# Kernel optimization log

Measured on AMD Instinct MI355X. Metric: run time of the kernel, lower is better.

The kernel has to match this reference:

```python
import jax, jax.numpy as jnp
import numpy as np

DIM = 2048
N_HEADS = 16
HEAD_DIM = DIM // N_HEADS
HIDDEN = 8192
BATCH = 2
SEQ = 2048
EPS = 1e-6


def setup_inputs() -> dict:
    key = jax.random.key(0)
    ks = jax.random.split(key, 10)
    x = jax.random.normal(ks[0], (BATCH, SEQ, DIM), dtype=jnp.float32)
    # standard RoPE angles: theta_j = 10000^{-2j/head_dim}, angle = pos * theta_j
    inv_freq = 1.0 / (10000.0 ** (np.arange(0, HEAD_DIM, 2, dtype=np.float32) / HEAD_DIM))
    angles = np.arange(SEQ, dtype=np.float32)[:, None] * inv_freq[None, :]  # [S, HD/2]
    freqs_cos = jnp.asarray(np.cos(angles))
    freqs_sin = jnp.asarray(np.sin(angles))
    # causal mask added to scores
    mask = jnp.where(jnp.tril(jnp.ones((SEQ, SEQ), dtype=bool)), 0.0, -jnp.inf)[None, None].astype(jnp.float32)
    s = 0.02
    wq = jax.random.normal(ks[1], (DIM, DIM), jnp.float32) * s
    wk = jax.random.normal(ks[2], (DIM, DIM), jnp.float32) * s
    wv = jax.random.normal(ks[3], (DIM, DIM), jnp.float32) * s
    wo = jax.random.normal(ks[4], (DIM, DIM), jnp.float32) * s
    w1 = jax.random.normal(ks[5], (DIM, HIDDEN), jnp.float32) * s
    w2 = jax.random.normal(ks[6], (HIDDEN, DIM), jnp.float32) * s
    w3 = jax.random.normal(ks[7], (DIM, HIDDEN), jnp.float32) * s
    attn_norm_w = jnp.ones((DIM,), jnp.float32)
    ffn_norm_w = jnp.ones((DIM,), jnp.float32)
    return {"x": x, "freqs_cos": freqs_cos, "freqs_sin": freqs_sin, "mask": mask,
            "wq": wq, "wk": wk, "wv": wv, "wo": wo, "w1": w1, "w2": w2, "w3": w3,
            "attn_norm_w": attn_norm_w, "ffn_norm_w": ffn_norm_w}


def _rmsnorm(x, w):
    xf = x.astype(jnp.float32)
    y = xf * jax.lax.rsqrt(jnp.mean(xf * xf, axis=-1, keepdims=True) + EPS)
    return y.astype(x.dtype) * w


def _rope(t, cos, sin):
    # t: [B,S,H,HD]; complex mult on adjacent pairs
    tr = t.astype(jnp.float32).reshape(*t.shape[:-1], HEAD_DIM // 2, 2)
    a, b = tr[..., 0], tr[..., 1]
    c = cos[None, :, None, :]  # [1,S,1,HD/2]
    s = sin[None, :, None, :]
    out = jnp.stack([a * c - b * s, a * s + b * c], axis=-1)
    return out.reshape(t.shape).astype(t.dtype)


def reference(x, freqs_cos, freqs_sin, mask, wq, wk, wv, wo, w1, w2, w3, attn_norm_w, ffn_norm_w):
    B, S, D = x.shape
    xn = _rmsnorm(x, attn_norm_w)
    q = (xn @ wq).reshape(B, S, N_HEADS, HEAD_DIM)
    k = (xn @ wk).reshape(B, S, N_HEADS, HEAD_DIM)
    v = (xn @ wv).reshape(B, S, N_HEADS, HEAD_DIM)
    q = _rope(q, freqs_cos, freqs_sin)
    k = _rope(k, freqs_cos, freqs_sin)
    scale = 1.0 / jnp.sqrt(jnp.float32(HEAD_DIM))
    scores = jnp.einsum('bqhd,bkhd->bhqk', q, k) * scale + mask
    probs = jax.nn.softmax(scores.astype(jnp.float32), axis=-1).astype(q.dtype)
    attn = jnp.einsum('bhqk,bkhd->bqhd', probs, v).reshape(B, S, D)
    h = x + attn @ wo
    hn = _rmsnorm(h, ffn_norm_w)
    ff = (jax.nn.silu(hn @ w1) * (hn @ w3)) @ w2
    return h + ff
```

## Files before the change

### kernel.cpp

```cpp
#include <hip/hip_runtime.h>
#include <cmath>

#define DIM    2048
#define NHEADS 16
#define HD     128
#define HIDDEN 8192
#define SEQ    2048
#define MTOK   4096
#define EPS    1e-6f

typedef __bf16 bf16;
typedef __bf16 bf16x8 __attribute__((ext_vector_type(8)));
typedef __bf16 bf16x4 __attribute__((ext_vector_type(4)));
typedef float  f32x4  __attribute__((ext_vector_type(4)));

typedef __attribute__((address_space(1))) const void gvoid_t;
typedef __attribute__((address_space(3))) void lvoid_t;

__global__ void k_transpose4(const float* __restrict__ in0, const float* __restrict__ in1,
                             const float* __restrict__ in2, const float* __restrict__ in3,
                             bf16* __restrict__ o0, bf16* __restrict__ o1,
                             bf16* __restrict__ o2, bf16* __restrict__ o3,
                             int R, int C) {
    __shared__ float tile[64][65];
    const float* in = blockIdx.z == 0 ? in0 : blockIdx.z == 1 ? in1 : blockIdx.z == 2 ? in2 : in3;
    bf16* out       = blockIdx.z == 0 ? o0  : blockIdx.z == 1 ? o1  : blockIdx.z == 2 ? o2  : o3;
    int r0 = blockIdx.y * 64, c0 = blockIdx.x * 64;
    int tx = threadIdx.x, ty = threadIdx.y;
#pragma unroll
    for (int i = ty; i < 64; i += 4)
        tile[i][tx] = in[(size_t)(r0 + i) * C + (c0 + tx)];
    __syncthreads();
#pragma unroll
    for (int i = ty; i < 64; i += 4)
        out[(size_t)(c0 + i) * R + (r0 + tx)] = (bf16)tile[tx][i];
}

__global__ void k_rmsnorm(const float* __restrict__ x, const float* __restrict__ w,
                          bf16* __restrict__ out) {
    int row = blockIdx.x;
    int tid = threadIdx.x;
    const float4* xr = (const float4*)(x + (size_t)row * DIM);
    float4 a = xr[tid];
    float4 b = xr[tid + 256];
    float ss = a.x*a.x + a.y*a.y + a.z*a.z + a.w*a.w
             + b.x*b.x + b.y*b.y + b.z*b.z + b.w*b.w;
#pragma unroll
    for (int off = 32; off > 0; off >>= 1) ss += __shfl_down(ss, off, 64);
    __shared__ float red[4];
    if ((tid & 63) == 0) red[tid >> 6] = ss;
    __syncthreads();
    float tot = red[0] + red[1] + red[2] + red[3];
    float inv = rsqrtf(tot * (1.0f / DIM) + EPS);
    const float4* wr = (const float4*)w;
    float4 w0 = wr[tid], w1 = wr[tid + 256];
    bf16x4* o = (bf16x4*)(out + (size_t)row * DIM);
    bf16x4 v0, v1;
    v0[0] = (bf16)(a.x * inv * w0.x); v0[1] = (bf16)(a.y * inv * w0.y);
    v0[2] = (bf16)(a.z * inv * w0.z); v0[3] = (bf16)(a.w * inv * w0.w);
    v1[0] = (bf16)(b.x * inv * w1.x); v1[1] = (bf16)(b.y * inv * w1.y);
    v1[2] = (bf16)(b.z * inv * w1.z); v1[3] = (bf16)(b.w * inv * w1.w);
    o[tid] = v0;
    o[tid + 256] = v1;
}

template<int CFG, int MODE>
__global__ __launch_bounds__(512, 2) void k2b(
    const bf16* __restrict__ A, const bf16* __restrict__ B1,
    const bf16* __restrict__ B2, const float* __restrict__ resid,
    const float* __restrict__ fcos, const float* __restrict__ fsin,
    bf16* __restrict__ oq, bf16* __restrict__ ok, bf16* __restrict__ ov,
    float* __restrict__ of, int N, int K)
{
    constexpr int  BN   = (CFG == 0) ? 256 : 128;
    constexpr int  WN   = (CFG == 0) ? 4 : 2;
    constexpr int  WM   = 8 / WN;
    constexpr int  MFR  = (256 / WM) / 16;
    constexpr bool DUAL = (CFG == 1);
    constexpr int  NH   = (CFG == 2) ? 3 : 4;
    constexpr uint32_t SLOT = (uint32_t)NH * 16384u;

    __shared__ __align__(16) char lds[2 * NH * 16384];

    const int tid  = threadIdx.x;
    const int wid  = tid >> 6;
    const int lane = tid & 63;
    const int quad = lane >> 4;
    const int l16  = lane & 15;
    const int wm   = wid / WN;
    const int wn   = wid % WN;
    const int m0   = blockIdx.y * 256;
    const int n0   = blockIdx.x * BN;
    const int NT   = K >> 6;

    const uint32_t swz0 = (uint32_t)((quad ^ (l16 & 7)) << 4);
    const uint32_t swz1 = (uint32_t)(((4 + quad) ^ (l16 & 7)) << 4);
    const uint32_t a_base  = (uint32_t)((wm * (256 / WM) + l16) * 128);
    const uint32_t b_base  = 32768u + (uint32_t)((wn * 64 + l16) * 128);

    auto stage = [&](int H, int Tt) {
        const uint32_t lb = (uint32_t)(Tt & 1) * SLOT + (uint32_t)H * 16384u
                          + (uint32_t)wid * 1024u;
        const int k0 = Tt << 6;
        const bf16* gb; int grow;
        if (H < 2) { gb = A; grow = m0 + H * 128; }
        else if constexpr (CFG == 0) { gb = B1; grow = n0 + (H - 2) * 128; }
        else if constexpr (CFG == 1) { gb = (H == 2) ? B1 : B2; grow = n0; }
        else { gb = B1; grow = n0; }
#pragma unroll
        for (int rho = 0; rho < 2; ++rho) {
            const int r  = (tid >> 3) + rho * 64;
            const int sp = (tid & 7) ^ (r & 7);
            const bf16* g = gb + (size_t)(grow + r) * K + k0 + sp * 8;
            __builtin_amdgcn_global_load_lds((gvoid_t*)g,
                (lvoid_t*)&lds[lb + (uint32_t)rho * 8192u], 16, 0, 0);
        }
    };

    f32x4 acc1[MFR][4] = {};
    f32x4 acc2[DUAL ? MFR : 1][4] = {};

#pragma unroll
    for (int h = 0; h < NH; ++h) stage(h, 0);
#pragma unroll
    for (int h = 0; h < NH; ++h) stage(h, 1);
    if constexpr (NH == 4) asm volatile("s_waitcnt vmcnt(8)" ::: "memory");
    else                   asm volatile("s_waitcnt vmcnt(6)" ::: "memory");
    __builtin_amdgcn_s_barrier();

    for (int T = 0; T < NT; ++T) {
        const uint32_t sb = (uint32_t)(T & 1) * SLOT;

#pragma unroll
        for (int ks = 0; ks < 2; ++ks) {
            const uint32_t sw = ks ? swz1 : swz0;
            bf16x8 af[MFR], bf1[4], bf2[DUAL ? 4 : 1];
#pragma unroll
            for (int mi = 0; mi < MFR; ++mi)
                af[mi] = *(const bf16x8*)&lds[sb + a_base + (uint32_t)mi * 2048u + sw];
#pragma unroll
            for (int ni = 0; ni < 4; ++ni)
                bf1[ni] = *(const bf16x8*)&lds[sb + b_base + (uint32_t)ni * 2048u + sw];
            if constexpr (DUAL)
#pragma unroll
                for (int ni = 0; ni < 4; ++ni)
                    bf2[ni] = *(const bf16x8*)&lds[sb + b_base + 16384u
                                                   + (uint32_t)ni * 2048u + sw];
            __builtin_amdgcn_s_setprio(1);
#pragma unroll
            for (int mi = 0; mi < MFR; ++mi)
#pragma unroll
                for (int ni = 0; ni < 4; ++ni) {
                    acc1[mi][ni] = __builtin_amdgcn_mfma_f32_16x16x32_bf16(
                        af[mi], bf1[ni], acc1[mi][ni], 0, 0, 0);
                    if constexpr (DUAL)
                        acc2[mi][ni] = __builtin_amdgcn_mfma_f32_16x16x32_bf16(
                            af[mi], bf2[ni], acc2[mi][ni], 0, 0, 0);
                }
            __builtin_amdgcn_s_setprio(0);
        }

        __builtin_amdgcn_s_barrier();

        if (T + 2 < NT) {
#pragma unroll
            for (int h = 0; h < NH; ++h) stage(h, T + 2);
        }
        if (T + 1 < NT) {
            if (T + 2 < NT) {
                if constexpr (NH == 4) asm volatile("s_waitcnt vmcnt(8)" ::: "memory");
                else                   asm volatile("s_waitcnt vmcnt(6)" ::: "memory");
            } else {
                asm volatile("s_waitcnt vmcnt(0)" ::: "memory");
            }
        }
        __builtin_amdgcn_s_barrier();
    }

    if constexpr (MODE == 1) {
        const int region = n0 >> 11;
        bf16* dst = region == 0 ? oq : (region == 1 ? ok : ov);
        const int c0 = (n0 & 2047) + wn * 64;
#pragma unroll
        for (int mi = 0; mi < MFR; ++mi)
#pragma unroll
            for (int i = 0; i < 4; ++i) {
                int row = m0 + wm * 128 + mi * 16 + quad * 4 + i;
                int pos = row & (SEQ - 1);
#pragma unroll
                for (int ni = 0; ni < 4; ++ni) {
                    int c = c0 + ni * 16 + l16;
                    float vA = acc1[mi][ni][i];
                    if (region < 2) {
                        float vB = __shfl_xor(vA, 1, 64);
                        int fi = (c & 127) >> 1;
                        float cs = fcos[pos * 64 + fi], sn = fsin[pos * 64 + fi];
                        vA = (l16 & 1) ? (vB * sn + vA * cs) : (vA * cs - vB * sn);
                    }
                    dst[(size_t)row * DIM + c] = (bf16)vA;
                }
            }
    } else if constexpr (MODE == 3) {
#pragma unroll
        for (int mi = 0; mi < MFR; ++mi)
#pragma unroll
            for (int i = 0; i < 4; ++i) {
                int row = m0 + wm * 64 + mi * 16 + quad * 4 + i;
#pragma unroll
                for (int ni = 0; ni < 4; ++ni) {
                    int col = n0 + wn * 64 + ni * 16 + l16;
                    float v1 = acc1[mi][ni][i];
                    float v2 = acc2[mi][ni][i];
                    float g = v1 / (1.0f + __expf(-v1));
                    oq[(size_t)row * (size_t)N + col] = (bf16)(g * v2);
                }
            }
    } else {
#pragma unroll
        for (int mi = 0; mi < MFR; ++mi)
#pragma unroll
            for (int i = 0; i < 4; ++i) {
                int row = m0 + wm * 64 + mi * 16 + quad * 4 + i;
#pragma unroll
                for (int ni = 0; ni < 4; ++ni) {
                    int col = n0 + wn * 64 + ni * 16 + l16;
                    of[(size_t)row * N + col] = resid[(size_t)row * N + col]
                                              + acc1[mi][ni][i];
                }
            }
    }
}

__global__ __launch_bounds__(256, 2) void k_flash(
    const bf16* __restrict__ q, const bf16* __restrict__ k,
    const bf16* __restrict__ v, bf16* __restrict__ o)
{
    const int qt = 15 - blockIdx.x;
    const int bh = blockIdx.y;
    const int b  = bh >> 4, h = bh & 15;
    const int tid  = threadIdx.x;
    const int wid  = tid >> 6, lane = tid & 63;
    const int quad = lane >> 4, l16 = lane & 15;

    __shared__ bf16 Ks [128][136];
    __shared__ bf16 Vts[128][136];

    const int q0 = qt * 128;
    const size_t baseQ  = ((size_t)b * SEQ + q0) * DIM + (size_t)h * HD;
    const size_t baseKV = ((size_t)b * SEQ) * DIM + (size_t)h * HD;

    bf16x8 qf[2][4];
#pragma unroll
    for (int mi = 0; mi < 2; ++mi)
#pragma unroll
        for (int ks = 0; ks < 4; ++ks)
            qf[mi][ks] = *(const bf16x8*)&q[baseQ +
                (size_t)(wid * 32 + mi * 16 + l16) * DIM + ks * 32 + quad * 8];

    f32x4 acc_o[2][8] = {};
    float m_run[2][4], l_run[2][4];
#pragma unroll
    for (int mi = 0; mi < 2; ++mi)
#pragma unroll
        for (int i = 0; i < 4; ++i) { m_run[mi][i] = -INFINITY; l_run[mi][i] = 0.f; }

    const float scale = 0.08838834764831845f;
    const int krow = tid >> 1, kcol = (tid & 1) * 64;

    for (int kt = 0; kt <= qt; ++kt) {
        const int kbase = kt * 128;
        __syncthreads();
#pragma unroll
        for (int j = 0; j < 8; ++j)
            *(uint4*)&Ks[krow][kcol + j * 8] =
                *(const uint4*)&k[baseKV + (size_t)(kbase + krow) * DIM + kcol + j * 8];
#pragma unroll
        for (int j = 0; j < 8; ++j) {
            bf16x8 vv = *(const bf16x8*)&v[baseKV + (size_t)(kbase + krow) * DIM + kcol + j * 8];
#pragma unroll
            for (int e = 0; e < 8; ++e)
                Vts[kcol + j * 8 + e][krow] = vv[e];
        }
        __syncthreads();

        f32x4 accs[2][8] = {};
#pragma unroll
        for (int ks = 0; ks < 4; ++ks)
#pragma unroll
            for (int ni = 0; ni < 8; ++ni) {
                bf16x8 kf = *(const bf16x8*)&Ks[ni * 16 + l16][ks * 32 + quad * 8];
#pragma unroll
                for (int mi = 0; mi < 2; ++mi)
                    accs[mi][ni] = __builtin_amdgcn_mfma_f32_16x16x32_bf16(
                        qf[mi][ks], kf, accs[mi][ni], 0, 0, 0);
            }

#pragma unroll
        for (int mi = 0; mi < 2; ++mi)
#pragma unroll
            for (int i = 0; i < 4; ++i) {
                int grow = q0 + wid * 32 + mi * 16 + quad * 4 + i;
                float mx = -INFINITY;
#pragma unroll
                for (int ni = 0; ni < 8; ++ni) {
                    float sv = accs[mi][ni][i] * scale;
                    int col = kbase + ni * 16 + l16;
                    if (col > grow) sv = -INFINITY;
                    accs[mi][ni][i] = sv;
                    mx = fmaxf(mx, sv);
                }
                mx = fmaxf(mx, __shfl_xor(mx, 1, 64));
                mx = fmaxf(mx, __shfl_xor(mx, 2, 64));
                mx = fmaxf(mx, __shfl_xor(mx, 4, 64));
                mx = fmaxf(mx, __shfl_xor(mx, 8, 64));
                float mnew  = fmaxf(m_run[mi][i], mx);
                float alpha = __expf(m_run[mi][i] - mnew);
                m_run[mi][i] = mnew;
                float rsum = 0.f;
#pragma unroll
                for (int ni = 0; ni < 8; ++ni) {
                    float p = __expf(accs[mi][ni][i] - mnew);
                    accs[mi][ni][i] = p;
                    rsum += p;
                }
                rsum += __shfl_xor(rsum, 1, 64);
                rsum += __shfl_xor(rsum, 2, 64);
                rsum += __shfl_xor(rsum, 4, 64);
                rsum += __shfl_xor(rsum, 8, 64);
                l_run[mi][i] = l_run[mi][i] * alpha + rsum;
#pragma unroll
                for (int ni = 0; ni < 8; ++ni) acc_o[mi][ni][i] *= alpha;
            }

        __syncthreads();
#pragma unroll
        for (int mi = 0; mi < 2; ++mi)
#pragma unroll
            for (int ni = 0; ni < 8; ++ni)
#pragma unroll
                for (int i = 0; i < 4; ++i)
                    Ks[wid * 32 + mi * 16 + quad * 4 + i][ni * 16 + l16] =
                        (bf16)accs[mi][ni][i];
        __syncthreads();

#pragma unroll
        for (int ks2 = 0; ks2 < 4; ++ks2) {
            bf16x8 pf[2];
#pragma unroll
            for (int mi = 0; mi < 2; ++mi)
                pf[mi] = *(const bf16x8*)&Ks[wid * 32 + mi * 16 + l16][ks2 * 32 + quad * 8];
#pragma unroll
            for (int ni = 0; ni < 8; ++ni) {
                bf16x8 vf = *(const bf16x8*)&Vts[ni * 16 + l16][ks2 * 32 + quad * 8];
#pragma unroll
                for (int mi = 0; mi < 2; ++mi)
                    acc_o[mi][ni] = __builtin_amdgcn_mfma_f32_16x16x32_bf16(
                        pf[mi], vf, acc_o[mi][ni], 0, 0, 0);
            }
        }
    }

#pragma unroll
    for (int mi = 0; mi < 2; ++mi)
#pragma unroll
        for (int i = 0; i < 4; ++i) {
            float invl = 1.0f / l_run[mi][i];
            int row = q0 + wid * 32 + mi * 16 + quad * 4 + i;
            size_t rb = ((size_t)b * SEQ + row) * DIM + (size_t)h * HD;
#pragma unroll
            for (int ni = 0; ni < 8; ++ni)
                o[rb + ni * 16 + l16] = (bf16)(acc_o[mi][ni][i] * invl);
        }
}

extern "C" void kernel_launch(void* const* d_in, const int* in_sizes, int n_in,
                              void* d_out, int out_size, void* d_ws, size_t ws_size,
                              hipStream_t stream)
{
    (void)in_sizes; (void)n_in; (void)out_size; (void)ws_size;
    const float* x    = (const float*)d_in[0];
    const float* fcos = (const float*)d_in[1];
    const float* fsin = (const float*)d_in[2];
    const float* wq   = (const float*)d_in[4];
    const float* wk   = (const float*)d_in[5];
    const float* wv   = (const float*)d_in[6];
    const float* wo   = (const float*)d_in[7];
    const float* w1   = (const float*)d_in[8];
    const float* w2   = (const float*)d_in[9];
    const float* w3   = (const float*)d_in[10];
    const float* anw  = (const float*)d_in[11];
    const float* fnw  = (const float*)d_in[12];
    float* out = (float*)d_out;

    char* ws = (char*)d_ws;
    size_t off = 0;
    auto alloc = [&](size_t bytes) { void* p = ws + off; off += (bytes + 255) & ~255ull; return p; };
    bf16* wqT = (bf16*)alloc((size_t)DIM * DIM * 2);
    bf16* wkT = (bf16*)alloc((size_t)DIM * DIM * 2);
    bf16* wvT = (bf16*)alloc((size_t)DIM * DIM * 2);
    bf16* woT = (bf16*)alloc((size_t)DIM * DIM * 2);
    bf16* w1T = (bf16*)alloc((size_t)HIDDEN * DIM * 2);
    bf16* w3T = (bf16*)alloc((size_t)HIDDEN * DIM * 2);
    bf16* xn  = (bf16*)alloc((size_t)MTOK * DIM * 2);
    bf16* qb  = (bf16*)alloc((size_t)MTOK * DIM * 2);
    bf16* kb  = (bf16*)alloc((size_t)MTOK * DIM * 2);
    bf16* vb  = (bf16*)alloc((size_t)MTOK * DIM * 2);
    bf16* ffb = (bf16*)alloc((size_t)MTOK * HIDDEN * 2);
    bf16* w2T = kb;

    dim3 tb(64, 4);
    k_transpose4<<<dim3(DIM / 64, DIM / 64, 4), tb, 0, stream>>>(
        wq, wk, wv, wo, wqT, wkT, wvT, woT, DIM, DIM);
    k_transpose4<<<dim3(HIDDEN / 64, DIM / 64, 2), tb, 0, stream>>>(
        w1, w3, nullptr, nullptr, w1T, w3T, nullptr, nullptr, DIM, HIDDEN);

    k_rmsnorm<<<MTOK, 256, 0, stream>>>(x, anw, xn);

    k2b<0, 1><<<dim3(3 * DIM / 256, MTOK / 256), 512, 0, stream>>>(
        xn, wqT, nullptr, nullptr, fcos, fsin, qb, kb, vb, nullptr, 3 * DIM, DIM);

    k_flash<<<dim3(SEQ / 128, 2 * NHEADS), 256, 0, stream>>>(qb, kb, vb, qb);

    k_transpose4<<<dim3(DIM / 64, HIDDEN / 64, 1), tb, 0, stream>>>(
        w2, nullptr, nullptr, nullptr, w2T, nullptr, nullptr, nullptr, HIDDEN, DIM);

    k2b<2, 2><<<dim3(DIM / 128, MTOK / 256), 512, 0, stream>>>(
        qb, woT, nullptr, x, nullptr, nullptr, nullptr, nullptr, nullptr, out, DIM, DIM);

    k_rmsnorm<<<MTOK, 256, 0, stream>>>(out, fnw, xn);

    k2b<1, 3><<<dim3(HIDDEN / 128, MTOK / 256), 512, 0, stream>>>(
        xn, w1T, w3T, nullptr, nullptr, nullptr, ffb, nullptr, nullptr, nullptr,
        HIDDEN, DIM);

    k2b<2, 2><<<dim3(DIM / 128, MTOK / 256), 512, 0, stream>>>(
        ffb, w2T, nullptr, out, nullptr, nullptr, nullptr, nullptr, nullptr, out,
        DIM, HIDDEN);
}
```

Before: 1.080 ms.

## Pre-transpose V for flash attention and shrink QKV GEMM tile to 256x128

```diff
diff --git a/kernel.cpp b/kernel.cpp
--- a/kernel.cpp
+++ b/kernel.cpp
@@ -34,6 +34,21 @@
 #pragma unroll
     for (int i = ty; i < 64; i += 4)
         out[(size_t)(c0 + i) * R + (r0 + tx)] = (bf16)tile[tx][i];
+}
+
+__global__ void k_transposeV(const bf16* __restrict__ v, bf16* __restrict__ vT) {
+    __shared__ bf16 t[64][66];
+    const int bh = blockIdx.z;
+    const int b  = bh >> 4, h = bh & 15;
+    const int s0 = blockIdx.x * 64, d0 = blockIdx.y * 64;
+    const int tx = threadIdx.x, ty = threadIdx.y;
+#pragma unroll
+    for (int i = ty; i < 64; i += 4)
+        t[i][tx] = v[((size_t)(b * SEQ + s0 + i)) * DIM + h * HD + d0 + tx];
+    __syncthreads();
+#pragma unroll
+    for (int i = ty; i < 64; i += 4)
+        vT[((size_t)(bh * HD + d0 + i)) * SEQ + s0 + tx] = t[tx][i];
 }
 
 __global__ void k_rmsnorm(const float* __restrict__ x, const float* __restrict__ w,
@@ -64,7 +79,7 @@
     o[tid + 256] = v1;
 }
 
-template<int CFG, int MODE>
+template<int DUALB, int MODE>
 __global__ __launch_bounds__(512, 2) void k2b(
     const bf16* __restrict__ A, const bf16* __restrict__ B1,
     const bf16* __restrict__ B2, const float* __restrict__ resid,
@@ -72,12 +87,8 @@
     bf16* __restrict__ oq, bf16* __restrict__ ok, bf16* __restrict__ ov,
     float* __restrict__ of, int N, int K)
 {
-    constexpr int  BN   = (CFG == 0) ? 256 : 128;
-    constexpr int  WN   = (CFG == 0) ? 4 : 2;
-    constexpr int  WM   = 8 / WN;
-    constexpr int  MFR  = (256 / WM) / 16;
-    constexpr bool DUAL = (CFG == 1);
-    constexpr int  NH   = (CFG == 2) ? 3 : 4;
+    constexpr int  MFR  = 4;
+    constexpr int  NH   = DUALB ? 4 : 3;
     constexpr uint32_t SLOT = (uint32_t)NH * 16384u;
 
     __shared__ __align__(16) char lds[2 * NH * 16384];
@@ -87,16 +98,16 @@
     const int lane = tid & 63;
     const int quad = lane >> 4;
     const int l16  = lane & 15;
-    const int wm   = wid / WN;
-    const int wn   = wid % WN;
+    const int wm   = wid >> 1;
+    const int wn   = wid & 1;
     const int m0   = blockIdx.y * 256;
-    const int n0   = blockIdx.x * BN;
+    const int n0   = blockIdx.x * 128;
     const int NT   = K >> 6;
 
     const uint32_t swz0 = (uint32_t)((quad ^ (l16 & 7)) << 4);
     const uint32_t swz1 = (uint32_t)(((4 + quad) ^ (l16 & 7)) << 4);
-    const uint32_t a_base  = (uint32_t)((wm * (256 / WM) + l16) * 128);
-    const uint32_t b_base  = 32768u + (uint32_t)((wn * 64 + l16) * 128);
+    const uint32_t a_base = (uint32_t)((wm * 64 + l16) * 128);
+    const uint32_t b_base = 32768u + (uint32_t)((wn * 64 + l16) * 128);
 
     auto stage = [&](int H, int Tt) {
         const uint32_t lb = (uint32_t)(Tt & 1) * SLOT + (uint32_t)H * 16384u
@@ -104,9 +115,8 @@
         const int k0 = Tt << 6;
         const bf16* gb; int grow;
         if (H < 2) { gb = A; grow = m0 + H * 128; }
-        else if constexpr (CFG == 0) { gb = B1; grow = n0 + (H - 2) * 128; }
-        else if constexpr (CFG == 1) { gb = (H == 2) ? B1 : B2; grow = n0; }
-        else { gb = B1; grow = n0; }
+        else if (H == 2) { gb = B1; grow = n0; }
+        else { gb = B2; grow = n0; }
 #pragma unroll
         for (int rho = 0; rho < 2; ++rho) {
             const int r  = (tid >> 3) + rho * 64;
@@ -118,7 +128,7 @@
     };
 
     f32x4 acc1[MFR][4] = {};
-    f32x4 acc2[DUAL ? MFR : 1][4] = {};
+    f32x4 acc2[DUALB ? MFR : 1][4] = {};
 
 #pragma unroll
     for (int h = 0; h < NH; ++h) stage(h, 0);
@@ -134,14 +144,14 @@
 #pragma unroll
         for (int ks = 0; ks < 2; ++ks) {
             const uint32_t sw = ks ? swz1 : swz0;
-            bf16x8 af[MFR], bf1[4], bf2[DUAL ? 4 : 1];
+            bf16x8 af[MFR], bf1[4], bf2[DUALB ? 4 : 1];
 #pragma unroll
             for (int mi = 0; mi < MFR; ++mi)
                 af[mi] = *(const bf16x8*)&lds[sb + a_base + (uint32_t)mi * 2048u + sw];
 #pragma unroll
             for (int ni = 0; ni < 4; ++ni)
                 bf1[ni] = *(const bf16x8*)&lds[sb + b_base + (uint32_t)ni * 2048u + sw];
-            if constexpr (DUAL)
+            if constexpr (DUALB)
 #pragma unroll
                 for (int ni = 0; ni < 4; ++ni)
                     bf2[ni] = *(const bf16x8*)&lds[sb + b_base + 16384u
@@ -153,7 +163,7 @@
                 for (int ni = 0; ni < 4; ++ni) {
                     acc1[mi][ni] = __builtin_amdgcn_mfma_f32_16x16x32_bf16(
                         af[mi], bf1[ni], acc1[mi][ni], 0, 0, 0);
-                    if constexpr (DUAL)
+                    if constexpr (DUALB)
                         acc2[mi][ni] = __builtin_amdgcn_mfma_f32_16x16x32_bf16(
                             af[mi], bf2[ni], acc2[mi][ni], 0, 0, 0);
                 }
@@ -185,7 +195,7 @@
         for (int mi = 0; mi < MFR; ++mi)
 #pragma unroll
             for (int i = 0; i < 4; ++i) {
-                int row = m0 + wm * 128 + mi * 16 + quad * 4 + i;
+                int row = m0 + wm * 64 + mi * 16 + quad * 4 + i;
                 int pos = row & (SEQ - 1);
 #pragma unroll
                 for (int ni = 0; ni < 4; ++ni) {
@@ -233,7 +243,7 @@
 
 __global__ __launch_bounds__(256, 2) void k_flash(
     const bf16* __restrict__ q, const bf16* __restrict__ k,
-    const bf16* __restrict__ v, bf16* __restrict__ o)
+    const bf16* __restrict__ vT, bf16* __restrict__ o)
 {
     const int qt = 15 - blockIdx.x;
     const int bh = blockIdx.y;
@@ -248,6 +258,7 @@
     const int q0 = qt * 128;
     const size_t baseQ  = ((size_t)b * SEQ + q0) * DIM + (size_t)h * HD;
     const size_t baseKV = ((size_t)b * SEQ) * DIM + (size_t)h * HD;
+    const size_t baseVT = (size_t)bh * HD * SEQ;
 
     bf16x8 qf[2][4];
 #pragma unroll
@@ -275,12 +286,9 @@
             *(uint4*)&Ks[krow][kcol + j * 8] =
                 *(const uint4*)&k[baseKV + (size_t)(kbase + krow) * DIM + kcol + j * 8];
 #pragma unroll
-        for (int j = 0; j < 8; ++j) {
-            bf16x8 vv = *(const bf16x8*)&v[baseKV + (size_t)(kbase + krow) * DIM + kcol + j * 8];
-#pragma unroll
-            for (int e = 0; e < 8; ++e)
-                Vts[kcol + j * 8 + e][krow] = vv[e];
-        }
+        for (int j = 0; j < 8; ++j)
+            *(uint4*)&Vts[krow][kcol + j * 8] =
+                *(const uint4*)&vT[baseVT + (size_t)krow * SEQ + kbase + kcol + j * 8];
         __syncthreads();
 
         f32x4 accs[2][8] = {};
@@ -407,6 +415,7 @@
     bf16* vb  = (bf16*)alloc((size_t)MTOK * DIM * 2);
     bf16* ffb = (bf16*)alloc((size_t)MTOK * HIDDEN * 2);
     bf16* w2T = kb;
+    bf16* vTb = ffb;
 
     dim3 tb(64, 4);
     k_transpose4<<<dim3(DIM / 64, DIM / 64, 4), tb, 0, stream>>>(
@@ -416,15 +425,17 @@
 
     k_rmsnorm<<<MTOK, 256, 0, stream>>>(x, anw, xn);
 
-    k2b<0, 1><<<dim3(3 * DIM / 256, MTOK / 256), 512, 0, stream>>>(
+    k2b<0, 1><<<dim3(3 * DIM / 128, MTOK / 256), 512, 0, stream>>>(
         xn, wqT, nullptr, nullptr, fcos, fsin, qb, kb, vb, nullptr, 3 * DIM, DIM);
 
-    k_flash<<<dim3(SEQ / 128, 2 * NHEADS), 256, 0, stream>>>(qb, kb, vb, qb);
+    k_transposeV<<<dim3(SEQ / 64, HD / 64, 2 * NHEADS), tb, 0, stream>>>(vb, vTb);
+
+    k_flash<<<dim3(SEQ / 128, 2 * NHEADS), 256, 0, stream>>>(qb, kb, vTb, qb);
 
     k_transpose4<<<dim3(DIM / 64, HIDDEN / 64, 1), tb, 0, stream>>>(
         w2, nullptr, nullptr, nullptr, w2T, nullptr, nullptr, nullptr, HIDDEN, DIM);
 
-    k2b<2, 2><<<dim3(DIM / 128, MTOK / 256), 512, 0, stream>>>(
+    k2b<0, 2><<<dim3(DIM / 128, MTOK / 256), 512, 0, stream>>>(
         qb, woT, nullptr, x, nullptr, nullptr, nullptr, nullptr, nullptr, out, DIM, DIM);
 
     k_rmsnorm<<<MTOK, 256, 0, stream>>>(out, fnw, xn);
@@ -433,7 +444,7 @@
         xn, w1T, w3T, nullptr, nullptr, nullptr, ffb, nullptr, nullptr, nullptr,
         HIDDEN, DIM);
 
-    k2b<2, 2><<<dim3(DIM / 128, MTOK / 256), 512, 0, stream>>>(
+    k2b<0, 2><<<dim3(DIM / 128, MTOK / 256), 512, 0, stream>>>(
         ffb, w2T, nullptr, out, nullptr, nullptr, nullptr, nullptr, nullptr, out,
         DIM, HIDDEN);
 }
```

New measurement: 1.057 ms. -2.1%, faster.
